# Optimization experiments

Hardware: AMD Instinct MI355X
Metric: run time of the kernel (lower is better)

Reference implementation:

```python
import jax, jax.numpy as jnp
import numpy as np

N = 150000   # nodes
E = 600000   # edges
F_IN = 32    # node features
H = 128      # hidden_channels == MLP_neurons
G = 2048     # graphs in batch


def setup_inputs() -> dict:
    key = jax.random.key(0)
    ks = iter(jax.random.split(key, 40))
    inp = {}
    inp['x'] = jax.random.normal(next(ks), (N, F_IN), dtype=jnp.float32)
    inp['edge_index'] = jax.random.randint(next(ks), (2, E), 0, N)
    inp['batch'] = jnp.sort(jax.random.randint(next(ks), (N,), 0, G))
    # GINConv MLPs: Linear(in,H) ReLU Linear(H,H) ReLU Linear(H,H)
    for i, f_in in enumerate([F_IN, H, H]):
        s1 = 1.0 / np.sqrt(f_in)
        s2 = 1.0 / np.sqrt(H)
        inp[f'c{i}_w1'] = jax.random.uniform(next(ks), (f_in, H), minval=-s1, maxval=s1)
        inp[f'c{i}_b1'] = jnp.zeros((H,), jnp.float32)
        inp[f'c{i}_w2'] = jax.random.uniform(next(ks), (H, H), minval=-s2, maxval=s2)
        inp[f'c{i}_b2'] = jnp.zeros((H,), jnp.float32)
        inp[f'c{i}_w3'] = jax.random.uniform(next(ks), (H, H), minval=-s2, maxval=s2)
        inp[f'c{i}_b3'] = jnp.zeros((H,), jnp.float32)
    s = 1.0 / np.sqrt(H)
    inp['fc0_w'] = jax.random.uniform(next(ks), (H, H), minval=-s, maxval=s)
    inp['fc0_b'] = jnp.zeros((H,), jnp.float32)
    inp['fc1_w'] = jax.random.uniform(next(ks), (H, H), minval=-s, maxval=s)
    inp['fc1_b'] = jnp.zeros((H,), jnp.float32)
    inp['out_w'] = jax.random.uniform(next(ks), (H, 2), minval=-s, maxval=s)
    inp['out_b'] = jnp.zeros((2,), jnp.float32)
    return inp


def _gin_layer(x, edge_index, w1, b1, w2, b2, w3, b3):
    # GINConv with eps=0: h = MLP(x + sum_{j in N(i)} x_j)
    agg = jax.ops.segment_sum(x[edge_index[0]], edge_index[1], num_segments=N)
    h = x + agg
    h = jax.nn.relu(h @ w1 + b1)
    h = jax.nn.relu(h @ w2 + b2)
    h = h @ w3 + b3
    return jax.nn.relu(h)  # outer .relu() in forward


def reference(x, edge_index, batch,
              c0_w1, c0_b1, c0_w2, c0_b2, c0_w3, c0_b3,
              c1_w1, c1_b1, c1_w2, c1_b2, c1_w3, c1_b3,
              c2_w1, c2_b1, c2_w2, c2_b2, c2_w3, c2_b3,
              fc0_w, fc0_b, fc1_w, fc1_b, out_w, out_b):
    h = _gin_layer(x, edge_index, c0_w1, c0_b1, c0_w2, c0_b2, c0_w3, c0_b3)
    h = _gin_layer(h, edge_index, c1_w1, c1_b1, c1_w2, c1_b2, c1_w3, c1_b3)
    h = _gin_layer(h, edge_index, c2_w1, c2_b1, c2_w2, c2_b2, c2_w3, c2_b3)
    # global_mean_pool over graph ids
    sums = jax.ops.segment_sum(h, batch, num_segments=G)            # [G,H]
    cnts = jax.ops.segment_sum(jnp.ones((N,), h.dtype), batch, num_segments=G)
    g = sums / jnp.maximum(cnts, 1.0)[:, None]
    # classifier head (dropout is identity at inference)
    g = jax.nn.relu(g @ fc0_w + fc0_b)
    g = jax.nn.relu(g @ fc1_w + fc1_b)
    return g @ out_w + out_b  # [G,2]
```

## Files before the change

kernel.cpp:

```cpp
#include <hip/hip_runtime.h>
#include <hip/hip_bf16.h>

#define NN 150000
#define EE 600000
#define F_IN 32
#define HD 128
#define GG 2048
#define CAP 28
#define NP 150016

typedef __attribute__((ext_vector_type(8))) short bf16x8;
typedef __attribute__((ext_vector_type(4))) float f32x4;
typedef __attribute__((ext_vector_type(4))) int i32x4;
typedef __attribute__((address_space(1))) const void g1void;
typedef __attribute__((address_space(3))) void l3void;

__device__ inline void split_bf16(float v, unsigned short& hi, unsigned short& lo) {
    __hip_bfloat16 h = __float2bfloat16(v);
    float hv = __bfloat162float(h);
    __hip_bfloat16 l = __float2bfloat16(v - hv);
    hi = *reinterpret_cast<unsigned short*>(&h);
    lo = *reinterpret_cast<unsigned short*>(&l);
}
__device__ inline unsigned short bf16_hi(float v) {
    __hip_bfloat16 h = __float2bfloat16(v);
    return *reinterpret_cast<unsigned short*>(&h);
}
__device__ inline float bf2f(unsigned short u) {
    union { unsigned int i; float f; } c;
    c.i = ((unsigned int)u) << 16;
    return c.f;
}

__global__ void init_zero(int* __restrict__ cnt_node, float* __restrict__ pooled) {
    int i = blockIdx.x * blockDim.x + threadIdx.x;
    if (i < NN) cnt_node[i] = 0;
    if (i < GG * HD) pooled[i] = 0.f;
}

__global__ void build_graph(const int* __restrict__ ei,
                            int* __restrict__ cnt_node,
                            int* __restrict__ bucket) {
    int e = blockIdx.x * blockDim.x + threadIdx.x;
    if (e >= EE) return;
    int src = ei[e];
    int dst = ei[EE + e];
    int slot = atomicAdd(&cnt_node[dst], 1);
    if (slot < CAP) bucket[dst * CAP + slot] = src;
}

struct PrepDesc { const float* src; unsigned short* dhi; unsigned short* dlo; int K; };
struct PrepArgs { PrepDesc d[9]; };

__global__ void prep_weights(PrepArgs pa) {
    PrepDesc de = pa.d[blockIdx.y];
    int total = de.K * HD;
    int KS = de.K >> 5;
    for (int idx = blockIdx.x * blockDim.x + threadIdx.x; idx < total;
         idx += gridDim.x * blockDim.x) {
        int k = idx / HD, h = idx - (idx / HD) * HD;
        unsigned short hi, lo;
        split_bf16(de.src[idx], hi, lo);
        int nt = h >> 4, m = h & 15;
        int ks = k >> 5, quad = (k >> 3) & 3, e = k & 7;
        int lane = quad * 16 + m;
        int pidx = ((nt * KS + ks) * 64 + lane) * 8 + e;
        de.dhi[pidx] = hi;
        de.dlo[pidx] = lo;
    }
}

template <int KS>
__device__ inline void stage_slice(const unsigned short* __restrict__ wh,
                                   const unsigned short* __restrict__ wl,
                                   int nt, unsigned short* dst, int wave, int lane) {
    if (KS == 4) {
        const unsigned short* gh = wh + nt * 2048 + wave * 512 + lane * 8;
        const unsigned short* gl = wl + nt * 2048 + wave * 512 + lane * 8;
        __builtin_amdgcn_global_load_lds((g1void*)gh, (l3void*)(dst + wave * 512), 16, 0, 0);
        __builtin_amdgcn_global_load_lds((g1void*)gl, (l3void*)(dst + 2048 + wave * 512), 16, 0, 0);
    } else {
        if (wave < 2) {
            const unsigned short* g = (wave == 0 ? wh : wl) + nt * 512 + lane * 8;
            __builtin_amdgcn_global_load_lds((g1void*)g, (l3void*)(dst + wave * 512), 16, 0, 0);
        }
    }
}

template <int K_IN, bool BF16IN, bool POOL>
__launch_bounds__(256, 2)
__global__ void gin_layer(const void* __restrict__ hin_,
                          const int* __restrict__ cnt_node,
                          const int* __restrict__ bucket,
                          const unsigned short* __restrict__ w1h, const unsigned short* __restrict__ w1l,
                          const float* __restrict__ b1,
                          const unsigned short* __restrict__ w2h, const unsigned short* __restrict__ w2l,
                          const float* __restrict__ b2,
                          const unsigned short* __restrict__ w3h, const unsigned short* __restrict__ w3l,
                          const float* __restrict__ b3,
                          unsigned short* __restrict__ out,
                          const int* __restrict__ batch,
                          float* __restrict__ pooled) {
    constexpr int KS1 = K_IN / 32;
    __shared__ unsigned int shp[4][2][16][128];
    __shared__ unsigned short ldsW[2][4096];

    const int wave = threadIdx.x >> 6;
    const int lane = threadIdx.x & 63;
    const int m = lane & 15;
    const int quad = lane >> 4;
    const int nodeBase = blockIdx.x * 128 + wave * 32;

    const float* hf = (const float*)hin_;
    const unsigned short* hb = (const unsigned short*)hin_;

    stage_slice<KS1>(w1h, w1l, 0, ldsW[0], wave, lane);

    int node_s[2], cnt_s[2];
#pragma unroll
    for (int s = 0; s < 2; s++) {
        int node = nodeBase + s * 16 + m;
        node_s[s] = node < NN ? node : NN - 1;
    }
    cnt_s[0] = cnt_node[node_s[0]];
    cnt_s[1] = cnt_node[node_s[1]];
#pragma unroll
    for (int s = 0; s < 2; s++) cnt_s[s] = cnt_s[s] < CAP ? cnt_s[s] : CAP;

    bf16x8 ah[2][KS1], al[2][KS1];
#pragma unroll
    for (int s = 0; s < 2; s++) {
        int node = node_s[s];
        float ag[KS1][8];
        if (BF16IN) {
            const unsigned short* rs = hb + (size_t)node * K_IN + quad * 8;
#pragma unroll
            for (int ks = 0; ks < KS1; ks++) {
                bf16x8 v = *(const bf16x8*)(rs + ks * 32);
#pragma unroll
                for (int e = 0; e < 8; e++) ag[ks][e] = bf2f((unsigned short)v[e]);
            }
        } else {
            const float* rs = hf + (size_t)node * K_IN + quad * 8;
#pragma unroll
            for (int ks = 0; ks < KS1; ks++) {
                float4 v0 = *(const float4*)(rs + ks * 32);
                float4 v1 = *(const float4*)(rs + ks * 32 + 4);
                ag[ks][0] = v0.x; ag[ks][1] = v0.y; ag[ks][2] = v0.z; ag[ks][3] = v0.w;
                ag[ks][4] = v1.x; ag[ks][5] = v1.y; ag[ks][6] = v1.z; ag[ks][7] = v1.w;
            }
        }
        int cnt = cnt_s[s];
        const int* b = bucket + (size_t)node * CAP;
        int i = 0;
        if (BF16IN) {
            if (cnt >= 4) {
                i32x4 iv = *(const i32x4*)b;
                for (; i + 4 <= cnt; i += 4) {
                    i32x4 ivn = *(const i32x4*)(b + i + 4);
                    bf16x8 v[4][KS1];
#pragma unroll
                    for (int j = 0; j < 4; j++) {
                        const unsigned short* r = hb + (size_t)iv[j] * K_IN + quad * 8;
#pragma unroll
                        for (int ks = 0; ks < KS1; ks++)
                            v[j][ks] = *(const bf16x8*)(r + ks * 32);
                    }
#pragma unroll
                    for (int ks = 0; ks < KS1; ks++)
#pragma unroll
                        for (int e = 0; e < 8; e++) {
                            float t01 = bf2f((unsigned short)v[0][ks][e]) +
                                        bf2f((unsigned short)v[1][ks][e]);
                            float t23 = bf2f((unsigned short)v[2][ks][e]) +
                                        bf2f((unsigned short)v[3][ks][e]);
                            ag[ks][e] += t01 + t23;
                        }
                    iv = ivn;
                }
            }
            for (; i < cnt; i++) {
                const unsigned short* r = hb + (size_t)b[i] * K_IN + quad * 8;
#pragma unroll
                for (int ks = 0; ks < KS1; ks++) {
                    bf16x8 v = *(const bf16x8*)(r + ks * 32);
#pragma unroll
                    for (int e = 0; e < 8; e++) ag[ks][e] += bf2f((unsigned short)v[e]);
                }
            }
        } else {
            for (; i + 8 <= cnt; i += 8) {
                float4 v0[8], v1[8];
#pragma unroll
                for (int j = 0; j < 8; j++) {
                    const float* r = hf + (size_t)b[i + j] * K_IN + quad * 8;
                    v0[j] = *(const float4*)r;
                    v1[j] = *(const float4*)(r + 4);
                }
#pragma unroll
                for (int e = 0; e < 4; e++) {
                    float s01 = (&v0[0].x)[e] + (&v0[1].x)[e] + (&v0[4].x)[e] + (&v0[5].x)[e];
                    float s23 = (&v0[2].x)[e] + (&v0[3].x)[e] + (&v0[6].x)[e] + (&v0[7].x)[e];
                    ag[0][e] += s01 + s23;
                }
#pragma unroll
                for (int e = 0; e < 4; e++) {
                    float s01 = (&v1[0].x)[e] + (&v1[1].x)[e] + (&v1[4].x)[e] + (&v1[5].x)[e];
                    float s23 = (&v1[2].x)[e] + (&v1[3].x)[e] + (&v1[6].x)[e] + (&v1[7].x)[e];
                    ag[0][e + 4] += s01 + s23;
                }
            }
            for (; i < cnt; i++) {
                const float* r = hf + (size_t)b[i] * K_IN + quad * 8;
                float4 v0 = *(const float4*)r;
                float4 v1 = *(const float4*)(r + 4);
                ag[0][0] += v0.x; ag[0][1] += v0.y; ag[0][2] += v0.z; ag[0][3] += v0.w;
                ag[0][4] += v1.x; ag[0][5] += v1.y; ag[0][6] += v1.z; ag[0][7] += v1.w;
            }
        }
#pragma unroll
        for (int ks = 0; ks < KS1; ks++) {
            bf16x8 vh, vl;
#pragma unroll
            for (int e = 0; e < 8; e++) {
                unsigned short hi, lo;
                split_bf16(ag[ks][e], hi, lo);
                vh[e] = (short)hi;
                vl[e] = (short)lo;
            }
            ah[s][ks] = vh;
            al[s][ks] = vl;
        }
    }

    bf16x8 a2h[2][4], a2l[2][4];
    const int fxm = (m & 7) << 2;

    __syncthreads();
#pragma unroll 1
    for (int nt = 0; nt < 8; nt++) {
        int cur = nt & 1;
        if (nt < 7) stage_slice<KS1>(w1h, w1l, nt + 1, ldsW[cur ^ 1], wave, lane);
        bf16x8 bh[KS1], bl[KS1];
#pragma unroll
        for (int ks = 0; ks < KS1; ks++) {
            bh[ks] = *(const bf16x8*)&ldsW[cur][(ks * 64 + lane) * 8];
            bl[ks] = *(const bf16x8*)&ldsW[cur][KS1 * 512 + (ks * 64 + lane) * 8];
        }
        f32x4 c0 = {0.f, 0.f, 0.f, 0.f};
        f32x4 c1 = {0.f, 0.f, 0.f, 0.f};
#pragma unroll
        for (int ks = 0; ks < KS1; ks++) {
            c0 = __builtin_amdgcn_mfma_f32_16x16x32_bf16(ah[0][ks], bh[ks], c0, 0, 0, 0);
            c1 = __builtin_amdgcn_mfma_f32_16x16x32_bf16(ah[1][ks], bh[ks], c1, 0, 0, 0);
            c0 = __builtin_amdgcn_mfma_f32_16x16x32_bf16(al[0][ks], bh[ks], c0, 0, 0, 0);
            c1 = __builtin_amdgcn_mfma_f32_16x16x32_bf16(al[1][ks], bh[ks], c1, 0, 0, 0);
            c0 = __builtin_amdgcn_mfma_f32_16x16x32_bf16(ah[0][ks], bl[ks], c0, 0, 0, 0);
            c1 = __builtin_amdgcn_mfma_f32_16x16x32_bf16(ah[1][ks], bl[ks], c1, 0, 0, 0);
        }
        float bj = b1[nt * 16 + m];
#pragma unroll
        for (int r = 0; r < 4; r++) {
            int row = quad * 4 + r;
            int col = (nt * 16 + m) ^ ((row & 7) << 2);
            unsigned short hi, lo;
            split_bf16(fmaxf(c0[r] + bj, 0.f), hi, lo);
            shp[wave][0][row][col] = (unsigned int)hi | ((unsigned int)lo << 16);
            split_bf16(fmaxf(c1[r] + bj, 0.f), hi, lo);
            shp[wave][1][row][col] = (unsigned int)hi | ((unsigned int)lo << 16);
        }
        __syncthreads();
    }
    stage_slice<4>(w2h, w2l, 0, ldsW[0], wave, lane);
#pragma unroll
    for (int s = 0; s < 2; s++)
#pragma unroll
        for (int ks = 0; ks < 4; ks++) {
            const unsigned int* rowp = &shp[wave][s][m][0];
            int base = ks * 32 + quad * 8;
            uint4 wa = *(const uint4*)&rowp[base ^ fxm];
            uint4 wb = *(const uint4*)&rowp[(base + 4) ^ fxm];
            union { unsigned int u[4]; bf16x8 v; } ch, cl;
            ch.u[0] = __builtin_amdgcn_perm(wa.y, wa.x, 0x05040100u);
            ch.u[1] = __builtin_amdgcn_perm(wa.w, wa.z, 0x05040100u);
            ch.u[2] = __builtin_amdgcn_perm(wb.y, wb.x, 0x05040100u);
            ch.u[3] = __builtin_amdgcn_perm(wb.w, wb.z, 0x05040100u);
            cl.u[0] = __builtin_amdgcn_perm(wa.y, wa.x, 0x07060302u);
            cl.u[1] = __builtin_amdgcn_perm(wa.w, wa.z, 0x07060302u);
            cl.u[2] = __builtin_amdgcn_perm(wb.y, wb.x, 0x07060302u);
            cl.u[3] = __builtin_amdgcn_perm(wb.w, wb.z, 0x07060302u);
            a2h[s][ks] = ch.v;
            a2l[s][ks] = cl.v;
        }
    __syncthreads();

#pragma unroll 1
    for (int nt = 0; nt < 8; nt++) {
        int cur = nt & 1;
        if (nt < 7) stage_slice<4>(w2h, w2l, nt + 1, ldsW[cur ^ 1], wave, lane);
        bf16x8 bh[4], bl[4];
#pragma unroll
        for (int ks = 0; ks < 4; ks++) {
            bh[ks] = *(const bf16x8*)&ldsW[cur][(ks * 64 + lane) * 8];
            bl[ks] = *(const bf16x8*)&ldsW[cur][2048 + (ks * 64 + lane) * 8];
        }
        f32x4 c0 = {0.f, 0.f, 0.f, 0.f};
        f32x4 c1 = {0.f, 0.f, 0.f, 0.f};
#pragma unroll
        for (int ks = 0; ks < 4; ks++) {
            c0 = __builtin_amdgcn_mfma_f32_16x16x32_bf16(a2h[0][ks], bh[ks], c0, 0, 0, 0);
            c1 = __builtin_amdgcn_mfma_f32_16x16x32_bf16(a2h[1][ks], bh[ks], c1, 0, 0, 0);
            c0 = __builtin_amdgcn_mfma_f32_16x16x32_bf16(a2l[0][ks], bh[ks], c0, 0, 0, 0);
            c1 = __builtin_amdgcn_mfma_f32_16x16x32_bf16(a2l[1][ks], bh[ks], c1, 0, 0, 0);
            c0 = __builtin_amdgcn_mfma_f32_16x16x32_bf16(a2h[0][ks], bl[ks], c0, 0, 0, 0);
            c1 = __builtin_amdgcn_mfma_f32_16x16x32_bf16(a2h[1][ks], bl[ks], c1, 0, 0, 0);
        }
        float bj = b2[nt * 16 + m];
#pragma unroll
        for (int r = 0; r < 4; r++) {
            int row = quad * 4 + r;
            int col = (nt * 16 + m) ^ ((row & 7) << 2);
            unsigned short hi, lo;
            split_bf16(fmaxf(c0[r] + bj, 0.f), hi, lo);
            shp[wave][0][row][col] = (unsigned int)hi | ((unsigned int)lo << 16);
            split_bf16(fmaxf(c1[r] + bj, 0.f), hi, lo);
            shp[wave][1][row][col] = (unsigned int)hi | ((unsigned int)lo << 16);
        }
        __syncthreads();
    }
    stage_slice<4>(w3h, w3l, 0, ldsW[0], wave, lane);
#pragma unroll
    for (int s = 0; s < 2; s++)
#pragma unroll
        for (int ks = 0; ks < 4; ks++) {
            const unsigned int* rowp = &shp[wave][s][m][0];
            int base = ks * 32 + quad * 8;
            uint4 wa = *(const uint4*)&rowp[base ^ fxm];
            uint4 wb = *(const uint4*)&rowp[(base + 4) ^ fxm];
            union { unsigned int u[4]; bf16x8 v; } ch, cl;
            ch.u[0] = __builtin_amdgcn_perm(wa.y, wa.x, 0x05040100u);
            ch.u[1] = __builtin_amdgcn_perm(wa.w, wa.z, 0x05040100u);
            ch.u[2] = __builtin_amdgcn_perm(wb.y, wb.x, 0x05040100u);
            ch.u[3] = __builtin_amdgcn_perm(wb.w, wb.z, 0x05040100u);
            cl.u[0] = __builtin_amdgcn_perm(wa.y, wa.x, 0x07060302u);
            cl.u[1] = __builtin_amdgcn_perm(wa.w, wa.z, 0x07060302u);
            cl.u[2] = __builtin_amdgcn_perm(wb.y, wb.x, 0x07060302u);
            cl.u[3] = __builtin_amdgcn_perm(wb.w, wb.z, 0x07060302u);
            a2h[s][ks] = ch.v;
            a2l[s][ks] = cl.v;
        }
    __syncthreads();

#pragma unroll 1
    for (int nt = 0; nt < 8; nt++) {
        int cur = nt & 1;
        if (nt < 7) stage_slice<4>(w3h, w3l, nt + 1, ldsW[cur ^ 1], wave, lane);
        bf16x8 bh[4], bl[4];
#pragma unroll
        for (int ks = 0; ks < 4; ks++) {
            bh[ks] = *(const bf16x8*)&ldsW[cur][(ks * 64 + lane) * 8];
            bl[ks] = *(const bf16x8*)&ldsW[cur][2048 + (ks * 64 + lane) * 8];
        }
        f32x4 c0 = {0.f, 0.f, 0.f, 0.f};
        f32x4 c1 = {0.f, 0.f, 0.f, 0.f};
#pragma unroll
        for (int ks = 0; ks < 4; ks++) {
            c0 = __builtin_amdgcn_mfma_f32_16x16x32_bf16(a2h[0][ks], bh[ks], c0, 0, 0, 0);
            c1 = __builtin_amdgcn_mfma_f32_16x16x32_bf16(a2h[1][ks], bh[ks], c1, 0, 0, 0);
            c0 = __builtin_amdgcn_mfma_f32_16x16x32_bf16(a2l[0][ks], bh[ks], c0, 0, 0, 0);
            c1 = __builtin_amdgcn_mfma_f32_16x16x32_bf16(a2l[1][ks], bh[ks], c1, 0, 0, 0);
            c0 = __builtin_amdgcn_mfma_f32_16x16x32_bf16(a2h[0][ks], bl[ks], c0, 0, 0, 0);
            c1 = __builtin_amdgcn_mfma_f32_16x16x32_bf16(a2h[1][ks], bl[ks], c1, 0, 0, 0);
        }
        float bj = b3[nt * 16 + m];
        if (POOL) {
            float* shf0 = (float*)&shp[wave][0][0][0];
            float* shf1 = (float*)&shp[wave][1][0][0];
#pragma unroll
            for (int r = 0; r < 4; r++) {
                int row = quad * 4 + r;
                int col = (nt * 16 + m) ^ ((row & 7) << 2);
                shf0[row * 128 + col] = fmaxf(c0[r] + bj, 0.f);
                shf1[row * 128 + col] = fmaxf(c1[r] + bj, 0.f);
            }
        } else {
            unsigned short* t0 = (unsigned short*)&shp[wave][0][0][0];
            unsigned short* t1 = (unsigned short*)&shp[wave][1][0][0];
#pragma unroll
            for (int r = 0; r < 4; r++) {
                int row = quad * 4 + r;
                int hh = nt * 16 + m;
                int w2 = (hh >> 1) ^ ((row & 7) << 2);
                t0[row * 256 + w2 * 2 + (hh & 1)] = bf16_hi(fmaxf(c0[r] + bj, 0.f));
                t1[row * 256 + w2 * 2 + (hh & 1)] = bf16_hi(fmaxf(c1[r] + bj, 0.f));
            }
        }
        __syncthreads();
    }

    if (POOL) {
#pragma unroll
        for (int h = 0; h < 2; h++) {
            float* shf = (float*)&shp[wave][h][0][0];
            int c0i = lane * 2;
            float run0 = 0.f, run1 = 0.f;
            int gp = -1;
            for (int rrow = 0; rrow < 16; rrow++) {
                int node = nodeBase + h * 16 + rrow;
                if (node >= NN) break;
                int g = batch[node];
                float2 xv = *(const float2*)&shf[rrow * 128 + (c0i ^ ((rrow & 7) << 2))];
                if (g != gp) {
                    if (gp >= 0) {
                        atomicAdd(&pooled[(size_t)gp * HD + c0i + 0], run0);
                        atomicAdd(&pooled[(size_t)gp * HD + c0i + 1], run1);
                    }
                    run0 = xv.x; run1 = xv.y; gp = g;
                } else {
                    run0 += xv.x; run1 += xv.y;
                }
            }
            if (gp >= 0) {
                atomicAdd(&pooled[(size_t)gp * HD + c0i + 0], run0);
                atomicAdd(&pooled[(size_t)gp * HD + c0i + 1], run1);
            }
        }
    } else {
#pragma unroll
        for (int s = 0; s < 2; s++) {
            unsigned short* sh16 = (unsigned short*)&shp[wave][s][0][0];
#pragma unroll
            for (int io = 0; io < 4; io++) {
                int row16 = io * 4 + quad;
                int wbase = (m * 4) ^ ((row16 & 7) << 2);
                int n2 = nodeBase + s * 16 + row16;
                bf16x8 v = *(const bf16x8*)&sh16[row16 * 256 + wbase * 2];
                if (n2 < NN) *(bf16x8*)&out[(size_t)n2 * HD + m * 8] = v;
            }
        }
    }
}

__device__ inline int lb_batch(const int* __restrict__ batch, int key) {
    int lo = 0, hi = NN;
    while (lo < hi) {
        int mid = (lo + hi) >> 1;
        if (batch[mid] < key) lo = mid + 1; else hi = mid;
    }
    return lo;
}

__launch_bounds__(128)
__global__ void head(const float* __restrict__ pooled, const int* __restrict__ batch,
                     const float* __restrict__ fc0_w, const float* __restrict__ fc0_b,
                     const float* __restrict__ fc1_w, const float* __restrict__ fc1_b,
                     const float* __restrict__ out_w, const float* __restrict__ out_b,
                     float* __restrict__ out) {
    int g = blockIdx.x;
    int j = threadIdx.x;
    __shared__ float s0[HD];
    __shared__ float s1[HD];
    int c = lb_batch(batch, g + 1) - lb_batch(batch, g);
    float cf = (float)(c > 1 ? c : 1);
    s0[j] = pooled[(size_t)g * HD + j] / cf;
    __syncthreads();

    float acc = fc0_b[j];
    for (int k = 0; k < HD; k += 4) {
        float4 hv = *(const float4*)&s0[k];
        acc = fmaf(hv.x, fc0_w[(k + 0) * HD + j], acc);
        acc = fmaf(hv.y, fc0_w[(k + 1) * HD + j], acc);
        acc = fmaf(hv.z, fc0_w[(k + 2) * HD + j], acc);
        acc = fmaf(hv.w, fc0_w[(k + 3) * HD + j], acc);
    }
    s1[j] = fmaxf(acc, 0.0f);
    __syncthreads();

    acc = fc1_b[j];
    for (int k = 0; k < HD; k += 4) {
        float4 hv = *(const float4*)&s1[k];
        acc = fmaf(hv.x, fc1_w[(k + 0) * HD + j], acc);
        acc = fmaf(hv.y, fc1_w[(k + 1) * HD + j], acc);
        acc = fmaf(hv.z, fc1_w[(k + 2) * HD + j], acc);
        acc = fmaf(hv.w, fc1_w[(k + 3) * HD + j], acc);
    }
    float v = fmaxf(acc, 0.0f);

    float p0 = v * out_w[j * 2 + 0];
    float p1 = v * out_w[j * 2 + 1];
    __syncthreads();
    s0[j] = p0;
    s1[j] = p1;
    __syncthreads();
    for (int off = 64; off >= 1; off >>= 1) {
        if (j < off) {
            s0[j] += s0[j + off];
            s1[j] += s1[j + off];
        }
        __syncthreads();
    }
    if (j == 0) {
        out[(size_t)g * 2 + 0] = s0[0] + out_b[0];
        out[(size_t)g * 2 + 1] = s1[0] + out_b[1];
    }
}

extern "C" void kernel_launch(void* const* d_in, const int* in_sizes, int n_in,
                              void* d_out, int out_size, void* d_ws, size_t ws_size,
                              hipStream_t stream) {
    const float* x     = (const float*)d_in[0];
    const int*   ei    = (const int*)d_in[1];
    const int*   batch = (const int*)d_in[2];
    const float* cw[3][6];
    for (int i = 0; i < 3; i++)
        for (int k = 0; k < 6; k++) cw[i][k] = (const float*)d_in[3 + 6 * i + k];
    const float* fc0_w = (const float*)d_in[21];
    const float* fc0_b = (const float*)d_in[22];
    const float* fc1_w = (const float*)d_in[23];
    const float* fc1_b = (const float*)d_in[24];
    const float* out_w = (const float*)d_in[25];
    const float* out_b = (const float*)d_in[26];
    float* out = (float*)d_out;

    char* ws = (char*)d_ws;
    size_t off = 0;
    auto carve = [&](size_t bytes) {
        void* p = ws + off;
        off += (bytes + 255) & ~(size_t)255;
        return p;
    };
    int*   cnt_node = (int*)carve((size_t)NN * 4);
    float* pooled   = (float*)carve((size_t)GG * HD * 4);
    int*   bucket   = (int*)carve((size_t)NN * CAP * 4 + 16);
    unsigned short* hA = (unsigned short*)carve((size_t)NP * HD * 2);
    unsigned short* hB = (unsigned short*)carve((size_t)NP * HD * 2);
    unsigned short* wHi[9];
    unsigned short* wLo[9];
    int wK[9] = {F_IN, HD, HD, HD, HD, HD, HD, HD, HD};
    for (int i = 0; i < 9; i++) {
        wHi[i] = (unsigned short*)carve((size_t)wK[i] * HD * 2);
        wLo[i] = (unsigned short*)carve((size_t)wK[i] * HD * 2);
    }
    (void)ws_size;

    init_zero<<<(GG * HD + 255) / 256, 256, 0, stream>>>(cnt_node, pooled);
    build_graph<<<(EE + 255) / 256, 256, 0, stream>>>(ei, cnt_node, bucket);

    PrepArgs pa;
    for (int l = 0; l < 3; l++)
        for (int s = 0; s < 3; s++) {
            int i = l * 3 + s;
            pa.d[i].src = cw[l][2 * s];
            pa.d[i].dhi = wHi[i];
            pa.d[i].dlo = wLo[i];
            pa.d[i].K = wK[i];
        }
    prep_weights<<<dim3(16, 9), 256, 0, stream>>>(pa);

    const int blocks = NP / 128;

    gin_layer<F_IN, false, false><<<blocks, 256, 0, stream>>>(x, cnt_node, bucket,
        wHi[0], wLo[0], cw[0][1], wHi[1], wLo[1], cw[0][3], wHi[2], wLo[2], cw[0][5],
        hA, batch, pooled);
    gin_layer<HD, true, false><<<blocks, 256, 0, stream>>>(hA, cnt_node, bucket,
        wHi[3], wLo[3], cw[1][1], wHi[4], wLo[4], cw[1][3], wHi[5], wLo[5], cw[1][5],
        hB, batch, pooled);
    gin_layer<HD, true, true><<<blocks, 256, 0, stream>>>(hB, cnt_node, bucket,
        wHi[6], wLo[6], cw[2][1], wHi[7], wLo[7], cw[2][3], wHi[8], wLo[8], cw[2][5],
        nullptr, batch, pooled);

    head<<<GG, 128, 0, stream>>>(pooled, batch, fc0_w, fc0_b, fc1_w, fc1_b, out_w, out_b, out);
}
```

Baseline: 477.2 us.

## Process node subtiles sequentially to halve LDS and raise occupancy

Each wave now runs the three MLP stages one 16-node subtile at a time instead of interleaving both subtiles. This halves the per-wave LDS staging buffer and lets launch bounds rise to three blocks per CU, aiming to hide gather latency with more resident waves. The cost is that every weight slice is staged twice and the number of block barriers doubles, with less MFMA interleaving per step. The vectorised prefetch of neighbor indices in the bf16 gather is also replaced by plain per-element index loads.

```diff
diff --git a/kernel.cpp b/kernel.cpp
--- a/kernel.cpp
+++ b/kernel.cpp
@@ -11,7 +11,6 @@
 
 typedef __attribute__((ext_vector_type(8))) short bf16x8;
 typedef __attribute__((ext_vector_type(4))) float f32x4;
-typedef __attribute__((ext_vector_type(4))) int i32x4;
 typedef __attribute__((address_space(1))) const void g1void;
 typedef __attribute__((address_space(3))) void l3void;
 
@@ -88,7 +87,7 @@
 }
 
 template <int K_IN, bool BF16IN, bool POOL>
-__launch_bounds__(256, 2)
+__launch_bounds__(256, 3)
 __global__ void gin_layer(const void* __restrict__ hin_,
                           const int* __restrict__ cnt_node,
                           const int* __restrict__ bucket,
@@ -102,7 +101,8 @@
                           const int* __restrict__ batch,
                           float* __restrict__ pooled) {
     constexpr int KS1 = K_IN / 32;
-    __shared__ unsigned int shp[4][2][16][128];
+    constexpr int UN = BF16IN ? 4 : 8;
+    __shared__ unsigned int shp[4][16][128];
     __shared__ unsigned short ldsW[2][4096];
 
     const int wave = threadIdx.x >> 6;
@@ -114,23 +114,11 @@
     const float* hf = (const float*)hin_;
     const unsigned short* hb = (const unsigned short*)hin_;
 
-    stage_slice<KS1>(w1h, w1l, 0, ldsW[0], wave, lane);
-
-    int node_s[2], cnt_s[2];
+    bf16x8 ah[2][KS1], al[2][KS1];
 #pragma unroll
     for (int s = 0; s < 2; s++) {
         int node = nodeBase + s * 16 + m;
-        node_s[s] = node < NN ? node : NN - 1;
-    }
-    cnt_s[0] = cnt_node[node_s[0]];
-    cnt_s[1] = cnt_node[node_s[1]];
-#pragma unroll
-    for (int s = 0; s < 2; s++) cnt_s[s] = cnt_s[s] < CAP ? cnt_s[s] : CAP;
-
-    bf16x8 ah[2][KS1], al[2][KS1];
-#pragma unroll
-    for (int s = 0; s < 2; s++) {
-        int node = node_s[s];
+        node = node < NN ? node : NN - 1;
         float ag[KS1][8];
         if (BF16IN) {
             const unsigned short* rs = hb + (size_t)node * K_IN + quad * 8;
@@ -142,42 +130,35 @@
             }
         } else {
             const float* rs = hf + (size_t)node * K_IN + quad * 8;
-#pragma unroll
-            for (int ks = 0; ks < KS1; ks++) {
-                float4 v0 = *(const float4*)(rs + ks * 32);
-                float4 v1 = *(const float4*)(rs + ks * 32 + 4);
-                ag[ks][0] = v0.x; ag[ks][1] = v0.y; ag[ks][2] = v0.z; ag[ks][3] = v0.w;
-                ag[ks][4] = v1.x; ag[ks][5] = v1.y; ag[ks][6] = v1.z; ag[ks][7] = v1.w;
-            }
-        }
-        int cnt = cnt_s[s];
+            float4 v0 = *(const float4*)rs;
+            float4 v1 = *(const float4*)(rs + 4);
+            ag[0][0] = v0.x; ag[0][1] = v0.y; ag[0][2] = v0.z; ag[0][3] = v0.w;
+            ag[0][4] = v1.x; ag[0][5] = v1.y; ag[0][6] = v1.z; ag[0][7] = v1.w;
+        }
+        int cnt = cnt_node[node];
+        cnt = cnt < CAP ? cnt : CAP;
         const int* b = bucket + (size_t)node * CAP;
         int i = 0;
         if (BF16IN) {
-            if (cnt >= 4) {
-                i32x4 iv = *(const i32x4*)b;
-                for (; i + 4 <= cnt; i += 4) {
-                    i32x4 ivn = *(const i32x4*)(b + i + 4);
-                    bf16x8 v[4][KS1];
-#pragma unroll
-                    for (int j = 0; j < 4; j++) {
-                        const unsigned short* r = hb + (size_t)iv[j] * K_IN + quad * 8;
-#pragma unroll
-                        for (int ks = 0; ks < KS1; ks++)
-                            v[j][ks] = *(const bf16x8*)(r + ks * 32);
+            for (; i + UN <= cnt; i += UN) {
+                bf16x8 v[UN][KS1];
+#pragma unroll
+                for (int j = 0; j < UN; j++) {
+                    const unsigned short* r = hb + (size_t)b[i + j] * K_IN + quad * 8;
+#pragma unroll
+                    for (int ks = 0; ks < KS1; ks++)
+                        v[j][ks] = *(const bf16x8*)(r + ks * 32);
+                }
+#pragma unroll
+                for (int ks = 0; ks < KS1; ks++)
+#pragma unroll
+                    for (int e = 0; e < 8; e++) {
+                        float t01 = bf2f((unsigned short)v[0][ks][e]) +
+                                    bf2f((unsigned short)v[1][ks][e]);
+                        float t23 = bf2f((unsigned short)v[2][ks][e]) +
+                                    bf2f((unsigned short)v[3][ks][e]);
+                        ag[ks][e] += t01 + t23;
                     }
-#pragma unroll
-                    for (int ks = 0; ks < KS1; ks++)
-#pragma unroll
-                        for (int e = 0; e < 8; e++) {
-                            float t01 = bf2f((unsigned short)v[0][ks][e]) +
-                                        bf2f((unsigned short)v[1][ks][e]);
-                            float t23 = bf2f((unsigned short)v[2][ks][e]) +
-                                        bf2f((unsigned short)v[3][ks][e]);
-                            ag[ks][e] += t01 + t23;
-                        }
-                    iv = ivn;
-                }
             }
             for (; i < cnt; i++) {
                 const unsigned short* r = hb + (size_t)b[i] * K_IN + quad * 8;
@@ -236,47 +217,43 @@
     bf16x8 a2h[2][4], a2l[2][4];
     const int fxm = (m & 7) << 2;
 
+    stage_slice<KS1>(w1h, w1l, 0, ldsW[0], wave, lane);
     __syncthreads();
+#pragma unroll
+    for (int s = 0; s < 2; s++) {
 #pragma unroll 1
-    for (int nt = 0; nt < 8; nt++) {
-        int cur = nt & 1;
-        if (nt < 7) stage_slice<KS1>(w1h, w1l, nt + 1, ldsW[cur ^ 1], wave, lane);
-        bf16x8 bh[KS1], bl[KS1];
-#pragma unroll
-        for (int ks = 0; ks < KS1; ks++) {
-            bh[ks] = *(const bf16x8*)&ldsW[cur][(ks * 64 + lane) * 8];
-            bl[ks] = *(const bf16x8*)&ldsW[cur][KS1 * 512 + (ks * 64 + lane) * 8];
-        }
-        f32x4 c0 = {0.f, 0.f, 0.f, 0.f};
-        f32x4 c1 = {0.f, 0.f, 0.f, 0.f};
-#pragma unroll
-        for (int ks = 0; ks < KS1; ks++) {
-            c0 = __builtin_amdgcn_mfma_f32_16x16x32_bf16(ah[0][ks], bh[ks], c0, 0, 0, 0);
-            c1 = __builtin_amdgcn_mfma_f32_16x16x32_bf16(ah[1][ks], bh[ks], c1, 0, 0, 0);
-            c0 = __builtin_amdgcn_mfma_f32_16x16x32_bf16(al[0][ks], bh[ks], c0, 0, 0, 0);
-            c1 = __builtin_amdgcn_mfma_f32_16x16x32_bf16(al[1][ks], bh[ks], c1, 0, 0, 0);
-            c0 = __builtin_amdgcn_mfma_f32_16x16x32_bf16(ah[0][ks], bl[ks], c0, 0, 0, 0);
-            c1 = __builtin_amdgcn_mfma_f32_16x16x32_bf16(ah[1][ks], bl[ks], c1, 0, 0, 0);
-        }
-        float bj = b1[nt * 16 + m];
-#pragma unroll
-        for (int r = 0; r < 4; r++) {
-            int row = quad * 4 + r;
-            int col = (nt * 16 + m) ^ ((row & 7) << 2);
-            unsigned short hi, lo;
-            split_bf16(fmaxf(c0[r] + bj, 0.f), hi, lo);
-            shp[wave][0][row][col] = (unsigned int)hi | ((unsigned int)lo << 16);
-            split_bf16(fmaxf(c1[r] + bj, 0.f), hi, lo);
-            shp[wave][1][row][col] = (unsigned int)hi | ((unsigned int)lo << 16);
-        }
-        __syncthreads();
-    }
-    stage_slice<4>(w2h, w2l, 0, ldsW[0], wave, lane);
-#pragma unroll
-    for (int s = 0; s < 2; s++)
+        for (int nt = 0; nt < 8; nt++) {
+            int t = s * 8 + nt;
+            int cur = t & 1;
+            if (t < 15) stage_slice<KS1>(w1h, w1l, (nt + 1) & 7, ldsW[cur ^ 1], wave, lane);
+            else        stage_slice<4>(w2h, w2l, 0, ldsW[cur ^ 1], wave, lane);
+            bf16x8 bh[KS1], bl[KS1];
+#pragma unroll
+            for (int ks = 0; ks < KS1; ks++) {
+                bh[ks] = *(const bf16x8*)&ldsW[cur][(ks * 64 + lane) * 8];
+                bl[ks] = *(const bf16x8*)&ldsW[cur][KS1 * 512 + (ks * 64 + lane) * 8];
+            }
+            f32x4 c = {0.f, 0.f, 0.f, 0.f};
+#pragma unroll
+            for (int ks = 0; ks < KS1; ks++) {
+                c = __builtin_amdgcn_mfma_f32_16x16x32_bf16(ah[s][ks], bh[ks], c, 0, 0, 0);
+                c = __builtin_amdgcn_mfma_f32_16x16x32_bf16(al[s][ks], bh[ks], c, 0, 0, 0);
+                c = __builtin_amdgcn_mfma_f32_16x16x32_bf16(ah[s][ks], bl[ks], c, 0, 0, 0);
+            }
+            float bj = b1[nt * 16 + m];
+#pragma unroll
+            for (int r = 0; r < 4; r++) {
+                int row = quad * 4 + r;
+                unsigned short hi, lo;
+                split_bf16(fmaxf(c[r] + bj, 0.f), hi, lo);
+                shp[wave][row][(nt * 16 + m) ^ ((row & 7) << 2)] =
+                    (unsigned int)hi | ((unsigned int)lo << 16);
+            }
+            __syncthreads();
+        }
 #pragma unroll
         for (int ks = 0; ks < 4; ks++) {
-            const unsigned int* rowp = &shp[wave][s][m][0];
+            const unsigned int* rowp = &shp[wave][m][0];
             int base = ks * 32 + quad * 8;
             uint4 wa = *(const uint4*)&rowp[base ^ fxm];
             uint4 wb = *(const uint4*)&rowp[(base + 4) ^ fxm];
@@ -292,48 +269,43 @@
             a2h[s][ks] = ch.v;
             a2l[s][ks] = cl.v;
         }
-    __syncthreads();
-
+    }
+
+#pragma unroll
+    for (int s = 0; s < 2; s++) {
 #pragma unroll 1
-    for (int nt = 0; nt < 8; nt++) {
-        int cur = nt & 1;
-        if (nt < 7) stage_slice<4>(w2h, w2l, nt + 1, ldsW[cur ^ 1], wave, lane);
-        bf16x8 bh[4], bl[4];
+        for (int nt = 0; nt < 8; nt++) {
+            int t = s * 8 + nt;
+            int cur = t & 1;
+            if (t < 15) stage_slice<4>(w2h, w2l, (nt + 1) & 7, ldsW[cur ^ 1], wave, lane);
+            else        stage_slice<4>(w3h, w3l, 0, ldsW[cur ^ 1], wave, lane);
+            bf16x8 bh[4], bl[4];
+#pragma unroll
+            for (int ks = 0; ks < 4; ks++) {
+                bh[ks] = *(const bf16x8*)&ldsW[cur][(ks * 64 + lane) * 8];
+                bl[ks] = *(const bf16x8*)&ldsW[cur][2048 + (ks * 64 + lane) * 8];
+            }
+            f32x4 c = {0.f, 0.f, 0.f, 0.f};
+#pragma unroll
+            for (int ks = 0; ks < 4; ks++) {
+                c = __builtin_amdgcn_mfma_f32_16x16x32_bf16(a2h[s][ks], bh[ks], c, 0, 0, 0);
+                c = __builtin_amdgcn_mfma_f32_16x16x32_bf16(a2l[s][ks], bh[ks], c, 0, 0, 0);
+                c = __builtin_amdgcn_mfma_f32_16x16x32_bf16(a2h[s][ks], bl[ks], c, 0, 0, 0);
+            }
+            float bj = b2[nt * 16 + m];
+#pragma unroll
+            for (int r = 0; r < 4; r++) {
+                int row = quad * 4 + r;
+                unsigned short hi, lo;
+                split_bf16(fmaxf(c[r] + bj, 0.f), hi, lo);
+                shp[wave][row][(nt * 16 + m) ^ ((row & 7) << 2)] =
+                    (unsigned int)hi | ((unsigned int)lo << 16);
+            }
+            __syncthreads();
+        }
 #pragma unroll
         for (int ks = 0; ks < 4; ks++) {
-            bh[ks] = *(const bf16x8*)&ldsW[cur][(ks * 64 + lane) * 8];
-            bl[ks] = *(const bf16x8*)&ldsW[cur][2048 + (ks * 64 + lane) * 8];
-        }
-        f32x4 c0 = {0.f, 0.f, 0.f, 0.f};
-        f32x4 c1 = {0.f, 0.f, 0.f, 0.f};
-#pragma unroll
-        for (int ks = 0; ks < 4; ks++) {
-            c0 = __builtin_amdgcn_mfma_f32_16x16x32_bf16(a2h[0][ks], bh[ks], c0, 0, 0, 0);
-            c1 = __builtin_amdgcn_mfma_f32_16x16x32_bf16(a2h[1][ks], bh[ks], c1, 0, 0, 0);
-            c0 = __builtin_amdgcn_mfma_f32_16x16x32_bf16(a2l[0][ks], bh[ks], c0, 0, 0, 0);
-            c1 = __builtin_amdgcn_mfma_f32_16x16x32_bf16(a2l[1][ks], bh[ks], c1, 0, 0, 0);
-            c0 = __builtin_amdgcn_mfma_f32_16x16x32_bf16(a2h[0][ks], bl[ks], c0, 0, 0, 0);
-            c1 = __builtin_amdgcn_mfma_f32_16x16x32_bf16(a2h[1][ks], bl[ks], c1, 0, 0, 0);
-        }
-        float bj = b2[nt * 16 + m];
-#pragma unroll
-        for (int r = 0; r < 4; r++) {
-            int row = quad * 4 + r;
-            int col = (nt * 16 + m) ^ ((row & 7) << 2);
-            unsigned short hi, lo;
-            split_bf16(fmaxf(c0[r] + bj, 0.f), hi, lo);
-            shp[wave][0][row][col] = (unsigned int)hi | ((unsigned int)lo << 16);
-            split_bf16(fmaxf(c1[r] + bj, 0.f), hi, lo);
-            shp[wave][1][row][col] = (unsigned int)hi | ((unsigned int)lo << 16);
-        }
-        __syncthreads();
-    }
-    stage_slice<4>(w3h, w3l, 0, ldsW[0], wave, lane);
-#pragma unroll
-    for (int s = 0; s < 2; s++)
-#pragma unroll
-        for (int ks = 0; ks < 4; ks++) {
-            const unsigned int* rowp = &shp[wave][s][m][0];
+            const unsigned int* rowp = &shp[wave][m][0];
             int base = ks * 32 + quad * 8;
             uint4 wa = *(const uint4*)&rowp[base ^ fxm];
             uint4 wb = *(const uint4*)&rowp[(base + 4) ^ fxm];
@@ -349,64 +321,57 @@
             a2h[s][ks] = ch.v;
             a2l[s][ks] = cl.v;
         }
-    __syncthreads();
-
+    }
+
+#pragma unroll
+    for (int s = 0; s < 2; s++) {
 #pragma unroll 1
-    for (int nt = 0; nt < 8; nt++) {
-        int cur = nt & 1;
-        if (nt < 7) stage_slice<4>(w3h, w3l, nt + 1, ldsW[cur ^ 1], wave, lane);
-        bf16x8 bh[4], bl[4];
-#pragma unroll
-        for (int ks = 0; ks < 4; ks++) {
-            bh[ks] = *(const bf16x8*)&ldsW[cur][(ks * 64 + lane) * 8];
-            bl[ks] = *(const bf16x8*)&ldsW[cur][2048 + (ks * 64 + lane) * 8];
-        }
-        f32x4 c0 = {0.f, 0.f, 0.f, 0.f};
-        f32x4 c1 = {0.f, 0.f, 0.f, 0.f};
-#pragma unroll
-        for (int ks = 0; ks < 4; ks++) {
-            c0 = __builtin_amdgcn_mfma_f32_16x16x32_bf16(a2h[0][ks], bh[ks], c0, 0, 0, 0);
-            c1 = __builtin_amdgcn_mfma_f32_16x16x32_bf16(a2h[1][ks], bh[ks], c1, 0, 0, 0);
-            c0 = __builtin_amdgcn_mfma_f32_16x16x32_bf16(a2l[0][ks], bh[ks], c0, 0, 0, 0);
-            c1 = __builtin_amdgcn_mfma_f32_16x16x32_bf16(a2l[1][ks], bh[ks], c1, 0, 0, 0);
-            c0 = __builtin_amdgcn_mfma_f32_16x16x32_bf16(a2h[0][ks], bl[ks], c0, 0, 0, 0);
-            c1 = __builtin_amdgcn_mfma_f32_16x16x32_bf16(a2h[1][ks], bl[ks], c1, 0, 0, 0);
-        }
-        float bj = b3[nt * 16 + m];
+        for (int nt = 0; nt < 8; nt++) {
+            int t = s * 8 + nt;
+            int cur = t & 1;
+            if (t < 15) stage_slice<4>(w3h, w3l, (nt + 1) & 7, ldsW[cur ^ 1], wave, lane);
+            bf16x8 bh[4], bl[4];
+#pragma unroll
+            for (int ks = 0; ks < 4; ks++) {
+                bh[ks] = *(const bf16x8*)&ldsW[cur][(ks * 64 + lane) * 8];
+                bl[ks] = *(const bf16x8*)&ldsW[cur][2048 + (ks * 64 + lane) * 8];
+            }
+            f32x4 c = {0.f, 0.f, 0.f, 0.f};
+#pragma unroll
+            for (int ks = 0; ks < 4; ks++) {
+                c = __builtin_amdgcn_mfma_f32_16x16x32_bf16(a2h[s][ks], bh[ks], c, 0, 0, 0);
+                c = __builtin_amdgcn_mfma_f32_16x16x32_bf16(a2l[s][ks], bh[ks], c, 0, 0, 0);
+                c = __builtin_amdgcn_mfma_f32_16x16x32_bf16(a2h[s][ks], bl[ks], c, 0, 0, 0);
+            }
+            float bj = b3[nt * 16 + m];
+            if (POOL) {
+                float* shf = (float*)&shp[wave][0][0];
+#pragma unroll
+                for (int r = 0; r < 4; r++) {
+                    int row = quad * 4 + r;
+                    shf[row * 128 + ((nt * 16 + m) ^ ((row & 7) << 2))] =
+                        fmaxf(c[r] + bj, 0.f);
+                }
+            } else {
+                unsigned short* sh16 = (unsigned short*)&shp[wave][0][0];
+#pragma unroll
+                for (int r = 0; r < 4; r++) {
+                    int row = quad * 4 + r;
+                    int hh = nt * 16 + m;
+                    int w2 = (hh >> 1) ^ ((row & 7) << 2);
+                    sh16[row * 256 + w2 * 2 + (hh & 1)] =
+                        bf16_hi(fmaxf(c[r] + bj, 0.f));
+                }
+            }
+            __syncthreads();
+        }
         if (POOL) {
-            float* shf0 = (float*)&shp[wave][0][0][0];
-            float* shf1 = (float*)&shp[wave][1][0][0];
-#pragma unroll
-            for (int r = 0; r < 4; r++) {
-                int row = quad * 4 + r;
-                int col = (nt * 16 + m) ^ ((row & 7) << 2);
-                shf0[row * 128 + col] = fmaxf(c0[r] + bj, 0.f);
-                shf1[row * 128 + col] = fmaxf(c1[r] + bj, 0.f);
-            }
-        } else {
-            unsigned short* t0 = (unsigned short*)&shp[wave][0][0][0];
-            unsigned short* t1 = (unsigned short*)&shp[wave][1][0][0];
-#pragma unroll
-            for (int r = 0; r < 4; r++) {
-                int row = quad * 4 + r;
-                int hh = nt * 16 + m;
-                int w2 = (hh >> 1) ^ ((row & 7) << 2);
-                t0[row * 256 + w2 * 2 + (hh & 1)] = bf16_hi(fmaxf(c0[r] + bj, 0.f));
-                t1[row * 256 + w2 * 2 + (hh & 1)] = bf16_hi(fmaxf(c1[r] + bj, 0.f));
-            }
-        }
-        __syncthreads();
-    }
-
-    if (POOL) {
-#pragma unroll
-        for (int h = 0; h < 2; h++) {
-            float* shf = (float*)&shp[wave][h][0][0];
+            float* shf = (float*)&shp[wave][0][0];
             int c0i = lane * 2;
             float run0 = 0.f, run1 = 0.f;
             int gp = -1;
             for (int rrow = 0; rrow < 16; rrow++) {
-                int node = nodeBase + h * 16 + rrow;
+                int node = nodeBase + s * 16 + rrow;
                 if (node >= NN) break;
                 int g = batch[node];
                 float2 xv = *(const float2*)&shf[rrow * 128 + (c0i ^ ((rrow & 7) << 2))];
@@ -424,11 +389,8 @@
                 atomicAdd(&pooled[(size_t)gp * HD + c0i + 0], run0);
                 atomicAdd(&pooled[(size_t)gp * HD + c0i + 1], run1);
             }
-        }
-    } else {
-#pragma unroll
-        for (int s = 0; s < 2; s++) {
-            unsigned short* sh16 = (unsigned short*)&shp[wave][s][0][0];
+        } else {
+            unsigned short* sh16 = (unsigned short*)&shp[wave][0][0];
 #pragma unroll
             for (int io = 0; io < 4; io++) {
                 int row16 = io * 4 + quad;
@@ -531,7 +493,7 @@
     };
     int*   cnt_node = (int*)carve((size_t)NN * 4);
     float* pooled   = (float*)carve((size_t)GG * HD * 4);
-    int*   bucket   = (int*)carve((size_t)NN * CAP * 4 + 16);
+    int*   bucket   = (int*)carve((size_t)NN * CAP * 4);
     unsigned short* hA = (unsigned short*)carve((size_t)NP * HD * 2);
     unsigned short* hB = (unsigned short*)carve((size_t)NP * HD * 2);
     unsigned short* wHi[9];
```

After: 445.7 us. 1.07x faster.
